# Optimization experiments

Measured on AMD Instinct MI355X. Metric: run time of the kernel, lower is better.

Reference implementation:

```python
import jax, jax.numpy as jnp
import numpy as np

IN_F = 4096
OUT_F = 4096
GS = 128  # group size for int4 scales


def setup_inputs() -> dict:
    key = jax.random.key(0)
    ks = jax.random.split(key, 5)
    x = jax.random.normal(ks[0], (4, 2048, IN_F), dtype=jnp.float32)
    # each byte packs two unsigned int4 values (low nibble = even col, high nibble = odd col)
    w_packed = jax.random.randint(ks[1], (OUT_F, IN_F // 2), 0, 256, dtype=jnp.int32)
    w_scales = jax.random.uniform(ks[2], (OUT_F, IN_F // GS), dtype=jnp.float32,
                                  minval=0.005, maxval=0.02)
    perm = jax.random.permutation(ks[3], IN_F).astype(jnp.int32)
    bias = jax.random.normal(ks[4], (OUT_F,), dtype=jnp.float32) * 0.01
    return {"x": x, "w_packed": w_packed, "w_scales": w_scales, "perm": perm, "bias": bias}


def _dequantize_groupwise_int4(w_packed, w_scales):
    # unpack two int4 values per byte, zero-point 8 -> symmetric range [-8, 7]
    low = (w_packed & 0xF) - 8
    high = ((w_packed >> 4) & 0xF) - 8
    q = jnp.stack([low, high], axis=-1).reshape(OUT_F, IN_F).astype(jnp.float32)
    # apply one scale per group of GS input features
    w = q.reshape(OUT_F, IN_F // GS, GS) * w_scales[:, :, None]
    return w.reshape(OUT_F, IN_F)  # [out_features, in_features]


def reference(x, w_packed, w_scales, perm, bias):
    shape = x.shape
    xf = x.reshape(-1, IN_F)[:, perm]          # activation permutation (GPTQ act-order)
    w = _dequantize_groupwise_int4(w_packed, w_scales)
    y = xf @ w.T                               # [tokens, out_features]
    return y.reshape(*shape[:-1], OUT_F) + bias
```

## Files before the change

### kernel.cpp

```cpp
#include <hip/hip_runtime.h>

#define IN_F 4096
#define OUT_F 4096
#define GS 128

#define BM 128
#define BN 128
#define BK 64

typedef int i32x4 __attribute__((ext_vector_type(4)));

typedef __attribute__((address_space(1))) void void_g;
typedef __attribute__((address_space(3))) void void_l;

__device__ __forceinline__ void async_copy16(void* lds, const void* g) {
  __builtin_amdgcn_global_load_lds((const void_g*)g, (void_l*)lds, 16, 0, 0);
}

__global__ void invperm_kernel(const int* __restrict__ perm, int* __restrict__ inv) {
  int i = blockIdx.x * blockDim.x + threadIdx.x;
  inv[perm[i]] = i;
}

__global__ __launch_bounds__(256) void xquant_kernel(
    const float* __restrict__ x,
    unsigned int* __restrict__ xq4,
    float* __restrict__ sx)
{
  __shared__ float red[256];
  const int t = blockIdx.x;
  const int tid = threadIdx.x;
  const float4* x4 = (const float4*)(x + (size_t)t * IN_F);

  float4 v[4];
  float m = 0.f;
#pragma unroll
  for (int i = 0; i < 4; ++i) {
    v[i] = x4[tid + i * 256];
    m = fmaxf(m, fmaxf(fmaxf(fabsf(v[i].x), fabsf(v[i].y)),
                       fmaxf(fabsf(v[i].z), fabsf(v[i].w))));
  }
  red[tid] = m;
  __syncthreads();
#pragma unroll
  for (int s = 128; s > 0; s >>= 1) {
    if (tid < s) red[tid] = fmaxf(red[tid], red[tid + s]);
    __syncthreads();
  }
  const float mx = red[0];
  const float r = 127.0f / mx;
  if (tid == 0) sx[t] = mx * (1.0f / 127.0f);

  unsigned int* orow = xq4 + (size_t)t * (IN_F / 4);
#pragma unroll
  for (int i = 0; i < 4; ++i) {
    int q0 = (int)rintf(v[i].x * r);
    int q1 = (int)rintf(v[i].y * r);
    int q2 = (int)rintf(v[i].z * r);
    int q3 = (int)rintf(v[i].w * r);
    orow[tid + i * 256] = (unsigned)(q0 & 0xFF) | ((unsigned)(q1 & 0xFF) << 8) |
                          ((unsigned)(q2 & 0xFF) << 16) | ((unsigned)(q3 & 0xFF) << 24);
  }
}

__global__ __launch_bounds__(256) void dequant_perm_kernel(
    const int* __restrict__ wp,
    const float* __restrict__ wsc,
    const int* __restrict__ inv,
    unsigned int* __restrict__ wq4,
    float* __restrict__ sw)
{
  __shared__ unsigned int prow[IN_F / 2];
  __shared__ float srow[IN_F / GS];
  __shared__ float red[256];
  const int o = blockIdx.x;
  const int tid = threadIdx.x;

  const int4* wp4 = (const int4*)(wp + (size_t)o * (IN_F / 2));
  int4* p4 = (int4*)prow;
#pragma unroll
  for (int i = 0; i < 2; ++i)
    p4[tid + i * 256] = wp4[tid + i * 256];
  if (tid < IN_F / GS) srow[tid] = wsc[o * (IN_F / GS) + tid];
  __syncthreads();

  float m = 0.f;
#pragma unroll
  for (int c = 0; c < 8; ++c) {
    const int p = tid + c * 256;
    const unsigned b = prow[p];
    const float s = srow[p >> 6];
    const float lo = (float)((int)(b & 0xFu) - 8);
    const float hi = (float)((int)((b >> 4) & 0xFu) - 8);
    m = fmaxf(m, fmaxf(fabsf(lo), fabsf(hi)) * s);
  }
  red[tid] = m;
  __syncthreads();
#pragma unroll
  for (int s = 128; s > 0; s >>= 1) {
    if (tid < s) red[tid] = fmaxf(red[tid], red[tid + s]);
    __syncthreads();
  }
  const float wmax = red[0];
  const float r = (wmax > 0.f) ? 127.0f / wmax : 0.f;
  if (tid == 0) sw[o] = wmax * (1.0f / 127.0f);

  unsigned int* orow = wq4 + (size_t)o * (IN_F / 4);
  const int4* inv4 = (const int4*)inv;
#pragma unroll
  for (int c = 0; c < 4; ++c) {
    const int p = tid + c * 256;
    const int4 iv = inv4[p];
    unsigned out = 0;
    const int idx[4] = {iv.x, iv.y, iv.z, iv.w};
#pragma unroll
    for (int e = 0; e < 4; ++e) {
      const int ii = idx[e];
      const unsigned wbits = prow[ii >> 1];
      const int n = (int)((wbits >> ((ii & 1) * 4)) & 0xFu) - 8;
      const float v = (float)n * srow[ii >> 7] * r;
      const int q = (int)rintf(v);
      out |= (unsigned)(q & 0xFF) << (e * 8);
    }
    orow[p] = out;
  }
}

__global__ __launch_bounds__(256) void gemm_kernel(
    const signed char* __restrict__ A,
    const signed char* __restrict__ B,
    const float* __restrict__ sx,
    const float* __restrict__ sw,
    const float* __restrict__ bias,
    float* __restrict__ C) {
  __shared__ signed char As[BM * BK];
  __shared__ signed char Bs[BN * BK];

  const int tid  = threadIdx.x;
  const int wave = tid >> 6;
  const int lane = tid & 63;
  const int quad = lane >> 4;
  const int l16  = lane & 15;

  const int bm = blockIdx.y;
  const int bn = blockIdx.x;

  const signed char* a_base = A + (size_t)bm * BM * IN_F;
  const signed char* b_base = B + (size_t)bn * BN * IN_F;

  const int srow_  = lane >> 2;
  const int schunk = lane & 3;

  i32x4 acc[4][4] = {};

  const int wm = (wave >> 1) * 64;
  const int wn = (wave & 1) * 64;

  for (int k0 = 0; k0 < IN_F; k0 += BK) {
#pragma unroll
    for (int c = 0; c < 2; ++c) {
      const int rblk = c * 4 + wave;
      const int grow = rblk * 16 + srow_;
      const size_t goff = (size_t)grow * IN_F + k0 + schunk * 16;
      async_copy16(&As[rblk * 16 * BK], a_base + goff);
      async_copy16(&Bs[rblk * 16 * BK], b_base + goff);
    }
    __syncthreads();

    i32x4 af[4], bfr[4];
#pragma unroll
    for (int i = 0; i < 4; ++i)
      af[i] = *(const i32x4*)&As[(wm + i * 16 + l16) * BK + quad * 16];
#pragma unroll
    for (int j = 0; j < 4; ++j)
      bfr[j] = *(const i32x4*)&Bs[(wn + j * 16 + l16) * BK + quad * 16];
#pragma unroll
    for (int i = 0; i < 4; ++i)
#pragma unroll
      for (int j = 0; j < 4; ++j)
        acc[i][j] = __builtin_amdgcn_mfma_i32_16x16x64_i8(af[i], bfr[j], acc[i][j], 0, 0, 0);
    __syncthreads();
  }

  float* sxs = (float*)As;
  float* sws = sxs + BM;
  float* bs  = sws + BN;
  if (tid < BM) {
    sxs[tid] = sx[bm * BM + tid];
  } else {
    const int c = tid - BM;
    sws[c] = sw[bn * BN + c];
    bs[c]  = bias[bn * BN + c];
  }
  __syncthreads();

  const int wm_g = bm * BM + wm;
  const int wn_g = bn * BN + wn;
#pragma unroll
  for (int j = 0; j < 4; ++j) {
    const int col_l = wn + j * 16 + l16;
    const float swv = sws[col_l];
    const float bv  = bs[col_l];
    const int col = wn_g + j * 16 + l16;
#pragma unroll
    for (int i = 0; i < 4; ++i) {
      const int row_l0 = wm + i * 16 + quad * 4;
      const int row0 = wm_g + i * 16 + quad * 4;
#pragma unroll
      for (int r = 0; r < 4; ++r)
        C[(size_t)(row0 + r) * OUT_F + col] =
            (float)acc[i][j][r] * (sxs[row_l0 + r] * swv) + bv;
    }
  }
}

extern "C" void kernel_launch(void* const* d_in, const int* in_sizes, int n_in,
                              void* d_out, int out_size, void* d_ws, size_t ws_size,
                              hipStream_t stream) {
  const float* x    = (const float*)d_in[0];
  const int*   wp   = (const int*)d_in[1];
  const float* wsc  = (const float*)d_in[2];
  const int*   perm = (const int*)d_in[3];
  const float* bias = (const float*)d_in[4];
  float* out = (float*)d_out;

  const int M = in_sizes[0] / IN_F;

  signed char* xq = (signed char*)d_ws;
  signed char* wq = xq + (size_t)M * IN_F;
  float* sx = (float*)(wq + (size_t)OUT_F * IN_F);
  float* sw = sx + M;
  int* inv = (int*)(sw + OUT_F);

  invperm_kernel<<<IN_F / 256, 256, 0, stream>>>(perm, inv);

  xquant_kernel<<<M, 256, 0, stream>>>(x, (unsigned int*)xq, sx);

  dequant_perm_kernel<<<OUT_F, 256, 0, stream>>>(wp, wsc, inv, (unsigned int*)wq, sw);

  dim3 grid(OUT_F / BN, M / BM);
  gemm_kernel<<<grid, 256, 0, stream>>>(xq, wq, sx, sw, bias, out);
}
```

Measured before the change: 431.1 us.

## Double-buffer int8 GEMM with 256x256 tiles, swizzled LDS, and fused prep kernel

The GEMM moves to 256x256 block tiles with a K step of 128 and 512 threads. It double-buffers LDS through async global-to-LDS copies spread across four sub-phases, with explicit waitcnt, barriers and setprio to overlap loads with MFMA work. LDS addresses are XOR-swizzled to reduce bank conflicts. The activation-quantize and weight-requantize kernels are merged into one launch. The aim is to hide memory latency and raise MFMA utilisation, at the cost of more registers and LDS (64KB for the buffers) and fragile hand-written wait counts.

Result: faster. 396.4 us (-8.1%).

```diff
diff --git a/kernel.cpp b/kernel.cpp
--- a/kernel.cpp
+++ b/kernel.cpp
@@ -4,9 +4,11 @@
 #define OUT_F 4096
 #define GS 128
 
-#define BM 128
-#define BN 128
-#define BK 64
+#define BM 256
+#define BN 256
+#define BKB 128
+#define NT (IN_F / BKB)
+#define BUFB (BM * BKB)
 
 typedef int i32x4 __attribute__((ext_vector_type(4)));
 
@@ -15,6 +17,13 @@
 
 __device__ __forceinline__ void async_copy16(void* lds, const void* g) {
   __builtin_amdgcn_global_load_lds((const void_g*)g, (void_l*)lds, 16, 0, 0);
+}
+
+__device__ __forceinline__ void stage_g(signed char* region, int rowbase,
+                                        const signed char* mat, int k0,
+                                        int wave, int growl, int gcolb) {
+  async_copy16(region + rowbase * BKB + wave * 1024,
+               mat + (size_t)(rowbase + growl) * IN_F + k0 + gcolb);
 }
 
 __global__ void invperm_kernel(const int* __restrict__ perm, int* __restrict__ inv) {
@@ -22,119 +31,184 @@
   inv[perm[i]] = i;
 }
 
-__global__ __launch_bounds__(256) void xquant_kernel(
+__global__ __launch_bounds__(256) void prep_kernel(
     const float* __restrict__ x,
     unsigned int* __restrict__ xq4,
-    float* __restrict__ sx)
-{
-  __shared__ float red[256];
-  const int t = blockIdx.x;
-  const int tid = threadIdx.x;
-  const float4* x4 = (const float4*)(x + (size_t)t * IN_F);
-
-  float4 v[4];
-  float m = 0.f;
-#pragma unroll
-  for (int i = 0; i < 4; ++i) {
-    v[i] = x4[tid + i * 256];
-    m = fmaxf(m, fmaxf(fmaxf(fabsf(v[i].x), fabsf(v[i].y)),
-                       fmaxf(fabsf(v[i].z), fabsf(v[i].w))));
-  }
-  red[tid] = m;
-  __syncthreads();
-#pragma unroll
-  for (int s = 128; s > 0; s >>= 1) {
-    if (tid < s) red[tid] = fmaxf(red[tid], red[tid + s]);
-    __syncthreads();
-  }
-  const float mx = red[0];
-  const float r = 127.0f / mx;
-  if (tid == 0) sx[t] = mx * (1.0f / 127.0f);
-
-  unsigned int* orow = xq4 + (size_t)t * (IN_F / 4);
-#pragma unroll
-  for (int i = 0; i < 4; ++i) {
-    int q0 = (int)rintf(v[i].x * r);
-    int q1 = (int)rintf(v[i].y * r);
-    int q2 = (int)rintf(v[i].z * r);
-    int q3 = (int)rintf(v[i].w * r);
-    orow[tid + i * 256] = (unsigned)(q0 & 0xFF) | ((unsigned)(q1 & 0xFF) << 8) |
-                          ((unsigned)(q2 & 0xFF) << 16) | ((unsigned)(q3 & 0xFF) << 24);
-  }
-}
-
-__global__ __launch_bounds__(256) void dequant_perm_kernel(
+    float* __restrict__ sx,
     const int* __restrict__ wp,
     const float* __restrict__ wsc,
     const int* __restrict__ inv,
     unsigned int* __restrict__ wq4,
-    float* __restrict__ sw)
+    float* __restrict__ sw,
+    int M)
 {
   __shared__ unsigned int prow[IN_F / 2];
   __shared__ float srow[IN_F / GS];
   __shared__ float red[256];
-  const int o = blockIdx.x;
   const int tid = threadIdx.x;
-
-  const int4* wp4 = (const int4*)(wp + (size_t)o * (IN_F / 2));
-  int4* p4 = (int4*)prow;
-#pragma unroll
-  for (int i = 0; i < 2; ++i)
-    p4[tid + i * 256] = wp4[tid + i * 256];
-  if (tid < IN_F / GS) srow[tid] = wsc[o * (IN_F / GS) + tid];
-  __syncthreads();
-
-  float m = 0.f;
-#pragma unroll
-  for (int c = 0; c < 8; ++c) {
-    const int p = tid + c * 256;
-    const unsigned b = prow[p];
-    const float s = srow[p >> 6];
-    const float lo = (float)((int)(b & 0xFu) - 8);
-    const float hi = (float)((int)((b >> 4) & 0xFu) - 8);
-    m = fmaxf(m, fmaxf(fabsf(lo), fabsf(hi)) * s);
-  }
-  red[tid] = m;
-  __syncthreads();
-#pragma unroll
-  for (int s = 128; s > 0; s >>= 1) {
-    if (tid < s) red[tid] = fmaxf(red[tid], red[tid + s]);
+  const int b = blockIdx.x;
+
+  if (b < M) {
+    const float4* x4 = (const float4*)(x + (size_t)b * IN_F);
+    float4 v[4];
+    float m = 0.f;
+#pragma unroll
+    for (int i = 0; i < 4; ++i) {
+      v[i] = x4[tid + i * 256];
+      m = fmaxf(m, fmaxf(fmaxf(fabsf(v[i].x), fabsf(v[i].y)),
+                         fmaxf(fabsf(v[i].z), fabsf(v[i].w))));
+    }
+    red[tid] = m;
     __syncthreads();
-  }
-  const float wmax = red[0];
-  const float r = (wmax > 0.f) ? 127.0f / wmax : 0.f;
-  if (tid == 0) sw[o] = wmax * (1.0f / 127.0f);
-
-  unsigned int* orow = wq4 + (size_t)o * (IN_F / 4);
-  const int4* inv4 = (const int4*)inv;
-#pragma unroll
-  for (int c = 0; c < 4; ++c) {
-    const int p = tid + c * 256;
-    const int4 iv = inv4[p];
-    unsigned out = 0;
-    const int idx[4] = {iv.x, iv.y, iv.z, iv.w};
-#pragma unroll
-    for (int e = 0; e < 4; ++e) {
-      const int ii = idx[e];
-      const unsigned wbits = prow[ii >> 1];
-      const int n = (int)((wbits >> ((ii & 1) * 4)) & 0xFu) - 8;
-      const float v = (float)n * srow[ii >> 7] * r;
-      const int q = (int)rintf(v);
-      out |= (unsigned)(q & 0xFF) << (e * 8);
-    }
-    orow[p] = out;
-  }
-}
-
-__global__ __launch_bounds__(256) void gemm_kernel(
+#pragma unroll
+    for (int s = 128; s > 0; s >>= 1) {
+      if (tid < s) red[tid] = fmaxf(red[tid], red[tid + s]);
+      __syncthreads();
+    }
+    const float mx = red[0];
+    const float r = 127.0f / mx;
+    if (tid == 0) sx[b] = mx * (1.0f / 127.0f);
+
+    unsigned int* orow = xq4 + (size_t)b * (IN_F / 4);
+#pragma unroll
+    for (int i = 0; i < 4; ++i) {
+      int q0 = (int)rintf(v[i].x * r);
+      int q1 = (int)rintf(v[i].y * r);
+      int q2 = (int)rintf(v[i].z * r);
+      int q3 = (int)rintf(v[i].w * r);
+      orow[tid + i * 256] = (unsigned)(q0 & 0xFF) | ((unsigned)(q1 & 0xFF) << 8) |
+                            ((unsigned)(q2 & 0xFF) << 16) | ((unsigned)(q3 & 0xFF) << 24);
+    }
+  } else {
+    const int o = b - M;
+    const int4* wp4 = (const int4*)(wp + (size_t)o * (IN_F / 2));
+    int4* p4 = (int4*)prow;
+#pragma unroll
+    for (int i = 0; i < 2; ++i)
+      p4[tid + i * 256] = wp4[tid + i * 256];
+    if (tid < IN_F / GS) srow[tid] = wsc[o * (IN_F / GS) + tid];
+    __syncthreads();
+
+    float m = 0.f;
+#pragma unroll
+    for (int c = 0; c < 8; ++c) {
+      const int p = tid + c * 256;
+      const unsigned bb = prow[p];
+      const float s = srow[p >> 6];
+      const float lo = (float)((int)(bb & 0xFu) - 8);
+      const float hi = (float)((int)((bb >> 4) & 0xFu) - 8);
+      m = fmaxf(m, fmaxf(fabsf(lo), fabsf(hi)) * s);
+    }
+    red[tid] = m;
+    __syncthreads();
+#pragma unroll
+    for (int s = 128; s > 0; s >>= 1) {
+      if (tid < s) red[tid] = fmaxf(red[tid], red[tid + s]);
+      __syncthreads();
+    }
+    const float wmax = red[0];
+    const float r = (wmax > 0.f) ? 127.0f / wmax : 0.f;
+    if (tid == 0) sw[o] = wmax * (1.0f / 127.0f);
+
+    unsigned int* orow = wq4 + (size_t)o * (IN_F / 4);
+    const int4* inv4 = (const int4*)inv;
+#pragma unroll
+    for (int c = 0; c < 4; ++c) {
+      const int p = tid + c * 256;
+      const int4 iv = inv4[p];
+      unsigned out = 0;
+      const int idx[4] = {iv.x, iv.y, iv.z, iv.w};
+#pragma unroll
+      for (int e = 0; e < 4; ++e) {
+        const int ii = idx[e];
+        const unsigned wbits = prow[ii >> 1];
+        const int n = (int)((wbits >> ((ii & 1) * 4)) & 0xFu) - 8;
+        const float v = (float)n * srow[ii >> 7] * r;
+        const int q = (int)rintf(v);
+        out |= (unsigned)(q & 0xFF) << (e * 8);
+      }
+      orow[p] = out;
+    }
+  }
+}
+
+template <bool LAST>
+__device__ __forceinline__ void gemm_tile(
+    const signed char* Ac, const signed char* Bc,
+    signed char* An, signed char* Bn,
+    const signed char* a_base, const signed char* b_base, int k0n,
+    int wave, int wm, int wn, int l16, int quad, int sx5,
+    int growl, int gcolb, i32x4 (&acc)[8][4])
+{
+  i32x4 bq[4][2];
+#pragma unroll
+  for (int p = 0; p < 4; ++p) {
+    if (p == 0) {
+#pragma unroll
+      for (int j = 0; j < 4; ++j)
+#pragma unroll
+        for (int ks = 0; ks < 2; ++ks) {
+          const int off = (((wn + j * 16 + l16) * BKB) + ks * 64 + quad * 16) ^ sx5;
+          bq[j][ks] = *(const i32x4*)(Bc + off);
+        }
+    }
+    i32x4 aq[2][2];
+#pragma unroll
+    for (int i = 0; i < 2; ++i)
+#pragma unroll
+      for (int ks = 0; ks < 2; ++ks) {
+        const int off = (((wm + p * 32 + i * 16 + l16) * BKB) + ks * 64 + quad * 16) ^ sx5;
+        aq[i][ks] = *(const i32x4*)(Ac + off);
+      }
+    if (!LAST) {
+      if (p == 0) {
+        stage_g(Bn, 0, b_base, k0n, wave, growl, gcolb);
+        stage_g(Bn, 64, b_base, k0n, wave, growl, gcolb);
+      } else if (p == 1) {
+        stage_g(Bn, 128, b_base, k0n, wave, growl, gcolb);
+        stage_g(Bn, 192, b_base, k0n, wave, growl, gcolb);
+      } else if (p == 2) {
+        stage_g(An, 0, a_base, k0n, wave, growl, gcolb);
+        stage_g(An, 128, a_base, k0n, wave, growl, gcolb);
+      } else {
+        stage_g(An, 64, a_base, k0n, wave, growl, gcolb);
+        stage_g(An, 192, a_base, k0n, wave, growl, gcolb);
+      }
+    }
+    __builtin_amdgcn_s_barrier();
+    asm volatile("s_waitcnt lgkmcnt(0)" ::: "memory");
+    __builtin_amdgcn_sched_barrier(0);
+    __builtin_amdgcn_s_setprio(1);
+#pragma unroll
+    for (int i = 0; i < 2; ++i)
+#pragma unroll
+      for (int j = 0; j < 4; ++j)
+#pragma unroll
+        for (int ks = 0; ks < 2; ++ks)
+          acc[2 * p + i][j] = __builtin_amdgcn_mfma_i32_16x16x64_i8(
+              aq[i][ks], bq[j][ks], acc[2 * p + i][j], 0, 0, 0);
+    __builtin_amdgcn_s_setprio(0);
+    if (p == 1) {
+      if (LAST) { asm volatile("s_waitcnt vmcnt(0)" ::: "memory"); }
+      else      { asm volatile("s_waitcnt vmcnt(4)" ::: "memory"); }
+      __builtin_amdgcn_sched_barrier(0);
+    } else if (p == 3 && !LAST) {
+      asm volatile("s_waitcnt vmcnt(2)" ::: "memory");
+      __builtin_amdgcn_sched_barrier(0);
+    }
+    __builtin_amdgcn_s_barrier();
+  }
+}
+
+__global__ __launch_bounds__(512, 2) void gemm_kernel(
     const signed char* __restrict__ A,
     const signed char* __restrict__ B,
     const float* __restrict__ sx,
     const float* __restrict__ sw,
     const float* __restrict__ bias,
     float* __restrict__ C) {
-  __shared__ signed char As[BM * BK];
-  __shared__ signed char Bs[BN * BK];
+  __shared__ signed char As[2 * BUFB];
+  __shared__ signed char Bs[2 * BUFB];
 
   const int tid  = threadIdx.x;
   const int wave = tid >> 6;
@@ -144,53 +218,53 @@
 
   const int bm = blockIdx.y;
   const int bn = blockIdx.x;
-
   const signed char* a_base = A + (size_t)bm * BM * IN_F;
   const signed char* b_base = B + (size_t)bn * BN * IN_F;
 
-  const int srow_  = lane >> 2;
-  const int schunk = lane & 3;
-
-  i32x4 acc[4][4] = {};
-
-  const int wm = (wave >> 1) * 64;
-  const int wn = (wave & 1) * 64;
-
-  for (int k0 = 0; k0 < IN_F; k0 += BK) {
-#pragma unroll
-    for (int c = 0; c < 2; ++c) {
-      const int rblk = c * 4 + wave;
-      const int grow = rblk * 16 + srow_;
-      const size_t goff = (size_t)grow * IN_F + k0 + schunk * 16;
-      async_copy16(&As[rblk * 16 * BK], a_base + goff);
-      async_copy16(&Bs[rblk * 16 * BK], b_base + goff);
-    }
-    __syncthreads();
-
-    i32x4 af[4], bfr[4];
-#pragma unroll
-    for (int i = 0; i < 4; ++i)
-      af[i] = *(const i32x4*)&As[(wm + i * 16 + l16) * BK + quad * 16];
-#pragma unroll
-    for (int j = 0; j < 4; ++j)
-      bfr[j] = *(const i32x4*)&Bs[(wn + j * 16 + l16) * BK + quad * 16];
-#pragma unroll
-    for (int i = 0; i < 4; ++i)
-#pragma unroll
-      for (int j = 0; j < 4; ++j)
-        acc[i][j] = __builtin_amdgcn_mfma_i32_16x16x64_i8(af[i], bfr[j], acc[i][j], 0, 0, 0);
-    __syncthreads();
-  }
+  const int wm = (wave >> 2) * 128;
+  const int wn = (wave & 3) * 64;
+  const int sx5 = ((l16 >> 2) & 1) << 5;
+
+  const int lt    = (tid << 4) ^ (((tid >> 5) & 1) << 5);
+  const int growl = lt >> 7;
+  const int gcolb = lt & 127;
+
+  i32x4 acc[8][4] = {};
+
+  stage_g(Bs, 0, b_base, 0, wave, growl, gcolb);
+  stage_g(Bs, 64, b_base, 0, wave, growl, gcolb);
+  stage_g(Bs, 128, b_base, 0, wave, growl, gcolb);
+  stage_g(Bs, 192, b_base, 0, wave, growl, gcolb);
+  stage_g(As, 0, a_base, 0, wave, growl, gcolb);
+  stage_g(As, 128, a_base, 0, wave, growl, gcolb);
+  stage_g(As, 64, a_base, 0, wave, growl, gcolb);
+  stage_g(As, 192, a_base, 0, wave, growl, gcolb);
+  asm volatile("s_waitcnt vmcnt(2)" ::: "memory");
+  __builtin_amdgcn_sched_barrier(0);
+  __builtin_amdgcn_s_barrier();
+
+#pragma unroll 1
+  for (int t = 0; t < NT - 1; ++t) {
+    const int cur = t & 1;
+    const int nxt = cur ^ 1;
+    gemm_tile<false>(As + cur * BUFB, Bs + cur * BUFB,
+                     As + nxt * BUFB, Bs + nxt * BUFB,
+                     a_base, b_base, (t + 1) * BKB,
+                     wave, wm, wn, l16, quad, sx5, growl, gcolb, acc);
+  }
+  gemm_tile<true>(As + ((NT - 1) & 1) * BUFB, Bs + ((NT - 1) & 1) * BUFB,
+                  nullptr, nullptr, a_base, b_base, 0,
+                  wave, wm, wn, l16, quad, sx5, growl, gcolb, acc);
 
   float* sxs = (float*)As;
   float* sws = sxs + BM;
-  float* bs  = sws + BN;
+  float* bsh = sws + BN;
   if (tid < BM) {
     sxs[tid] = sx[bm * BM + tid];
   } else {
     const int c = tid - BM;
     sws[c] = sw[bn * BN + c];
-    bs[c]  = bias[bn * BN + c];
+    bsh[c] = bias[bn * BN + c];
   }
   __syncthreads();
 
@@ -200,10 +274,10 @@
   for (int j = 0; j < 4; ++j) {
     const int col_l = wn + j * 16 + l16;
     const float swv = sws[col_l];
-    const float bv  = bs[col_l];
+    const float bv  = bsh[col_l];
     const int col = wn_g + j * 16 + l16;
 #pragma unroll
-    for (int i = 0; i < 4; ++i) {
+    for (int i = 0; i < 8; ++i) {
       const int row_l0 = wm + i * 16 + quad * 4;
       const int row0 = wm_g + i * 16 + quad * 4;
 #pragma unroll
@@ -234,10 +308,9 @@
 
   invperm_kernel<<<IN_F / 256, 256, 0, stream>>>(perm, inv);
 
-  xquant_kernel<<<M, 256, 0, stream>>>(x, (unsigned int*)xq, sx);
-
-  dequant_perm_kernel<<<OUT_F, 256, 0, stream>>>(wp, wsc, inv, (unsigned int*)wq, sw);
+  prep_kernel<<<M + OUT_F, 256, 0, stream>>>(
+      x, (unsigned int*)xq, sx, wp, wsc, inv, (unsigned int*)wq, sw, M);
 
   dim3 grid(OUT_F / BN, M / BM);
-  gemm_kernel<<<grid, 256, 0, stream>>>(xq, wq, sx, sw, bias, out);
-}
+  gemm_kernel<<<grid, 512, 0, stream>>>(xq, wq, sx, sw, bias, out);
+}
```
